# Optimization experiments

Measured on AMD Instinct MI355X. Metric: run time of the kernel, lower is better.

Reference implementation:

```python
import jax, jax.numpy as jnp
import numpy as np

H, B, N, D = 8, 256, 200, 128
KD = D // H                      # key_dim = embed_dim // n_heads = 16
TRI = N * (N - 1) // 2           # strictly upper-triangular count per matrix
NORM = 1.0 / np.sqrt(KD)
NEG = -jnp.inf


def setup_inputs() -> dict:
    key = jax.random.key(0)
    k1, k2, k3, k4, k5 = jax.random.split(key, 5)
    q = jax.random.normal(k1, (B, N, D), dtype=jnp.float32)
    che_mask = jax.random.randint(k2, (H, B, TRI), 0, 2).astype(bool)
    exchange = jax.random.randint(k3, (B, 2), 0, N)
    stdv = 1.0 / np.sqrt(KD)
    Wq = jax.random.uniform(k4, (H, D, KD), jnp.float32, -stdv, stdv)
    Wk = jax.random.uniform(k5, (H, D, KD), jnp.float32, -stdv, stdv)
    return {"q": q, "che_mask": che_mask, "exchange": exchange, "Wq": Wq, "Wk": Wk}


def reference(q, che_mask, exchange, Wq, Wk):
    # Q, K: (H, B, N, KD)
    Q = jnp.einsum('bnd,hdk->hbnk', q, Wq)
    K = jnp.einsum('bnd,hdk->hbnk', q, Wk)
    # tanh-rescaled scores: (H, B, N, N)
    comp = jnp.tanh(NORM * jnp.einsum('hbik,hbjk->hbij', Q, K)) * 10.0

    # 1) lower triangle (incl. diagonal) -> -inf
    tril = jnp.tril(jnp.ones((N, N), dtype=bool))
    comp = jnp.where(tril, NEG, comp)

    # 2) strictly-upper positions where che_mask == 0 -> -inf
    # torch boolean indexing enumerates ~tril elements row-major == triu_indices order
    iu0, iu1 = np.triu_indices(N, k=1)
    keep = jnp.zeros((H, B, N, N), dtype=bool).at[:, :, iu0, iu1].set(che_mask)
    comp = jnp.where(jnp.logical_and(~tril, ~keep), NEG, comp)

    # 3) last 28 query rows fully masked
    comp = comp.at[:, :, -28:, :].set(NEG)

    # 4) per-batch exchange-pair scatter on head 0 only
    b_idx = jnp.arange(B)
    comp = comp.at[0, b_idx, exchange[:, 1], exchange[:, 0]].set(NEG)
    comp = comp.at[0, b_idx, exchange[:, 0], exchange[:, 1]].set(NEG)

    # 5) fixed column 100 masked
    comp = comp.at[:, :, :, 100].set(NEG)

    # global (flattened over N*N) softmax / log_softmax per (head, batch)
    im = comp.reshape(H, B, N * N)
    return jax.nn.log_softmax(im, axis=-1), jax.nn.softmax(im, axis=-1)
```

## Files before the change

### kernel.cpp

```cpp
#include <hip/hip_runtime.h>
#include <math.h>

#define Hh 8
#define Bb 256
#define Nn 200
#define Dd 128
#define KDk 16
#define TRI_ 19900
#define NN_ 40000
#define OUT_HALF 81920000ull
#define QK_FLOATS 6553600

#define NEG_FIN (-1.0e30f)

__device__ __forceinline__ float fast_exp2(float x) {
#if __has_builtin(__builtin_amdgcn_exp2f)
  return __builtin_amdgcn_exp2f(x);
#else
  return exp2f(x);
#endif
}
__device__ __forceinline__ float fast_log2(float x) {
#if __has_builtin(__builtin_amdgcn_logf)
  return __builtin_amdgcn_logf(x);
#else
  return log2f(x);
#endif
}
__device__ __forceinline__ float fast_rcp(float x) {
#if __has_builtin(__builtin_amdgcn_rcpf)
  return __builtin_amdgcn_rcpf(x);
#else
  return 1.0f / x;
#endif
}

__device__ __forceinline__ float dot16(float4 a0, float4 a1, float4 a2, float4 a3,
                                       float4 b0, float4 b1, float4 b2, float4 b3) {
  return a0.x*b0.x + a0.y*b0.y + a0.z*b0.z + a0.w*b0.w
       + a1.x*b1.x + a1.y*b1.y + a1.z*b1.z + a1.w*b1.w
       + a2.x*b2.x + a2.y*b2.y + a2.z*b2.z + a2.w*b2.w
       + a3.x*b3.x + a3.y*b3.y + a3.z*b3.z + a3.w*b3.w;
}

__global__ void k_detect(const unsigned char* __restrict__ che, int* __restrict__ flag) {
  const int t = threadIdx.x;
  unsigned char a4 = 0, a8 = 0;
  #pragma unroll
  for (int k = 0; k < 16; ++k) {
    const int i = t * 16 + k;
    const unsigned char v = che[i];
    if (i & 3) a4 |= v;
    else if (i & 7) a8 |= v;
  }
  const unsigned long long m4 = __ballot(a4 != 0);
  const unsigned long long m8 = __ballot(a8 != 0);
  if (t == 0) *flag = m4 ? 1 : (m8 ? 4 : 8);
}

__global__ __launch_bounds__(256) void k_proj(const float* __restrict__ q,
    const float* __restrict__ Wq, const float* __restrict__ Wk,
    float* __restrict__ Qg, float* __restrict__ Kg) {
  __shared__ float As[64 * 132];
  __shared__ float Bst[128 * 68];
  const int tid = threadIdx.x;
  const int r0 = blockIdx.x * 64;
  const int c0 = blockIdx.y * 64;

  const float4* src = (const float4*)q;
  #pragma unroll
  for (int p = 0; p < 8; ++p) {
    const int t2 = tid + p * 256;
    const int row = t2 >> 5, q4 = t2 & 31;
    float4 v = src[(size_t)(r0 + row) * 32 + q4];
    *(float4*)&As[row * 132 + q4 * 4] = v;
  }
  #pragma unroll
  for (int p = 0; p < 32; ++p) {
    const int t2 = tid + p * 256;
    const int d = t2 >> 6, cl = t2 & 63;
    const int c = c0 + cl;
    const int h = c >> 5, m = (c >> 4) & 1, kk = c & 15;
    const float* Wsrc = m ? Wk : Wq;
    Bst[d * 68 + cl] = Wsrc[(h * 128 + d) * 16 + kk];
  }
  __syncthreads();

  const int tn = tid >> 4;
  const int tc = tid & 15;
  float acc[4][4] = {};
  #pragma unroll
  for (int dq = 0; dq < 32; ++dq) {
    float a[4][4];
    #pragma unroll
    for (int r = 0; r < 4; ++r) {
      float4 t = *(const float4*)&As[(tn * 4 + r) * 132 + dq * 4];
      a[r][0] = t.x; a[r][1] = t.y; a[r][2] = t.z; a[r][3] = t.w;
    }
    #pragma unroll
    for (int dd = 0; dd < 4; ++dd) {
      float4 bv = *(const float4*)&Bst[(dq * 4 + dd) * 68 + tc * 4];
      #pragma unroll
      for (int r = 0; r < 4; ++r) {
        acc[r][0] += a[r][dd] * bv.x;
        acc[r][1] += a[r][dd] * bv.y;
        acc[r][2] += a[r][dd] * bv.z;
        acc[r][3] += a[r][dd] * bv.w;
      }
    }
  }
  const int cq = c0 + tc * 4;
  const int h = cq >> 5, m = (cq >> 4) & 1, kkb = cq & 15;
  float* dst = m ? Kg : Qg;
  #pragma unroll
  for (int r = 0; r < 4; ++r) {
    const int nrow = r0 + tn * 4 + r;
    const int b = nrow / 200, n = nrow - b * 200;
    float4 v = make_float4(acc[r][0], acc[r][1], acc[r][2], acc[r][3]);
    *(float4*)(dst + (size_t)((h * 256 + b) * 200 + n) * 16 + kkb) = v;
  }
}

__global__ __launch_bounds__(512, 4) void k_attn(
    const float* __restrict__ Qg, const float* __restrict__ Kg,
    const unsigned char* __restrict__ che, const int* __restrict__ exch,
    const int* __restrict__ flag, float* __restrict__ out) {
  const int hb = blockIdx.x;
  const int h = hb >> 8, b = hb & 255;
  const int tid = threadIdx.x;
  const int lane = tid & 63;
  const int wave = __builtin_amdgcn_readfirstlane(tid >> 6);
  const int i0 = wave * 25;
  const float* __restrict__ Qb = Qg + (size_t)hb * 3200;
  const float* __restrict__ Kb = Kg + (size_t)hb * 3200;
  const int cs = *flag;
  const unsigned char* __restrict__ cheB = che + (size_t)hb * TRI_ * (size_t)cs;
  const int e0 = exch[2 * b], e1 = exch[2 * b + 1];
  const int h0 = (h == 0) ? 1 : 0;

  __shared__ float red[8];
  __shared__ float c3lds[8 * 25 * 8];

  const float C2E = 0.72134752044448f;
  const float L2E = 1.44269504088896f;

  float acc[25][3];
  #pragma unroll
  for (int c = 0; c < 3; ++c) {
    const int j = lane + (c << 6);
    const float4* kp = (const float4*)(Kb + j * 16);
    const float4 k0 = kp[0], k1 = kp[1], k2 = kp[2], k3 = kp[3];
    #pragma unroll
    for (int r = 0; r < 25; ++r) {
      const float4* qp = (const float4*)(Qb + (i0 + r) * 16);
      acc[r][c] = dot16(qp[0], qp[1], qp[2], qp[3], k0, k1, k2, k3);
    }
  }
  const int j3 = 192 + (lane & 7);
  const float4* kp3 = (const float4*)(Kb + j3 * 16);
  const float4 k30 = kp3[0], k31 = kp3[1], k32 = kp3[2], k33 = kp3[3];

  float psum = 0.0f;
  #pragma unroll
  for (int r = 0; r < 25; ++r) {
    const int i = i0 + r;
    const int rowv = (i < 172) ? 1 : 0;
    const int base = i * 199 - ((i * (i - 1)) >> 1) - i - 1;
    #pragma unroll
    for (int c = 0; c < 4; ++c) {
      int j; float d;
      if (c < 3) {
        j = lane + (c << 6);
        d = acc[r][c];
      } else {
        j = j3;
        const float4* qp = (const float4*)(Qb + i * 16);
        d = dot16(qp[0], qp[1], qp[2], qp[3], k30, k31, k32, k33);
      }
      int geo = rowv & ((j > i) ? 1 : 0) & ((j != 100) ? 1 : 0);
      if (c == 3) geo &= (lane < 8) ? 1 : 0;
      const int idx = geo ? (base + j) : 0;
      const unsigned char mb = cheB[(size_t)idx * (size_t)cs];
      int valid = geo & ((mb != 0) ? 1 : 0);
      const int exhit = (((i == e1) & (j == e0)) | ((i == e0) & (j == e1))) ? 1 : 0;
      valid &= (h0 & exhit) ^ 1;
      const float E = fast_exp2(C2E * d);
      const float rc = fast_rcp(E + 1.0f);
      const float s10 = valid ? (-20.0f * rc) : NEG_FIN;
      psum += fast_exp2(L2E * s10);
      if (c < 3) acc[r][c] = s10;
      else if (lane < 8) c3lds[wave * 200 + r * 8 + lane] = s10;
    }
  }

  #pragma unroll
  for (int o = 32; o > 0; o >>= 1) psum += __shfl_xor(psum, o, 64);
  if (lane == 0) red[wave] = psum;
  __syncthreads();
  float Z = 0.0f;
  #pragma unroll
  for (int w2 = 0; w2 < 8; ++w2) Z += red[w2];
  const float lnZ = 0.69314718056f * fast_log2(Z);

  const size_t obase = (size_t)hb * NN_;
  float* __restrict__ oLS = out + obase;
  float* __restrict__ oSM = out + OUT_HALF + obase;
  #pragma unroll
  for (int r = 0; r < 25; ++r) {
    const int ro = (i0 + r) * 200;
    #pragma unroll
    for (int c = 0; c < 3; ++c) {
      const int j = lane + (c << 6);
      const float ls = acc[r][c] - lnZ;
      const float sm = fast_exp2(L2E * ls);
      oLS[ro + j] = ls;
      oSM[ro + j] = sm;
    }
    {
      const float s10 = c3lds[wave * 200 + r * 8 + (lane & 7)];
      const float ls = s10 - lnZ;
      const float sm = fast_exp2(L2E * ls);
      if (lane < 8) {
        oLS[ro + j3] = ls;
        oSM[ro + j3] = sm;
      }
    }
  }
}

extern "C" void kernel_launch(void* const* d_in, const int* in_sizes, int n_in,
                              void* d_out, int out_size, void* d_ws, size_t ws_size,
                              hipStream_t stream) {
  const float* q           = (const float*)d_in[0];
  const unsigned char* che = (const unsigned char*)d_in[1];
  const int* exch          = (const int*)d_in[2];
  const float* Wq          = (const float*)d_in[3];
  const float* Wk          = (const float*)d_in[4];
  float* out = (float*)d_out;
  float* ws  = (float*)d_ws;

  const size_t need = (size_t)(4 + 2 * QK_FLOATS) * sizeof(float);
  int* flag = (int*)ws;
  float* Qg = ws + 4;
  float* Kg = Qg + QK_FLOATS;

  if (ws_size < need) {
    k_detect<<<dim3(1), dim3(64), 0, stream>>>(che, flag);
    return;
  }

  k_detect<<<dim3(1), dim3(64), 0, stream>>>(che, flag);
  k_proj<<<dim3(800, 4), dim3(256), 0, stream>>>(q, Wq, Wk, Qg, Kg);
  k_attn<<<dim3(2048), dim3(512), 0, stream>>>(Qg, Kg, che, exch, flag, out);
}
```

Measured before the change: 1.087 ms.

## Compute only live upper-triangle segments via work table and store masked regions directly

Replaces the per-wave row blocks with a compile-time table of (row, 64-column segment) work items covering only the strictly upper triangle of the 172 live rows. Dot products, tanh and mask reads now run only for those items, and the lower triangle and dead rows are written as constants. The block grows to 16 waves of 1024 threads and outputs use nontemporal stores. In exchange, the Q/K dot products are recomputed per item instead of reusing register tiles, and the larger block may lower occupancy.

```diff
diff --git a/kernel.cpp b/kernel.cpp
--- a/kernel.cpp
+++ b/kernel.cpp
@@ -13,6 +13,10 @@
 
 #define NEG_FIN (-1.0e30f)
 
+#define NITEMS 385
+#define NWAVES 16
+#define ITEMS_PER_WAVE 25
+
 __device__ __forceinline__ float fast_exp2(float x) {
 #if __has_builtin(__builtin_amdgcn_exp2f)
   return __builtin_amdgcn_exp2f(x);
@@ -42,6 +46,20 @@
        + a2.x*b2.x + a2.y*b2.y + a2.z*b2.z + a2.w*b2.w
        + a3.x*b3.x + a3.y*b3.y + a3.z*b3.z + a3.w*b3.w;
 }
+
+struct ItemTab { unsigned int v[NWAVES * ITEMS_PER_WAVE]; };
+static constexpr ItemTab make_tab() {
+  ItemTab t{};
+  int n = 0;
+  for (int i = 0; i < 172; ++i) {
+    int len = 199 - i;
+    int g = (len + 63) >> 6;
+    for (int k = 0; k < g; ++k) { t.v[n] = (unsigned int)((i << 2) | k); ++n; }
+  }
+  for (; n < NWAVES * ITEMS_PER_WAVE; ++n) t.v[n] = 0xFFFFu;
+  return t;
+}
+__constant__ ItemTab d_tab = make_tab();
 
 __global__ void k_detect(const unsigned char* __restrict__ che, int* __restrict__ flag) {
   const int t = threadIdx.x;
@@ -121,7 +139,7 @@
   }
 }
 
-__global__ __launch_bounds__(512, 4) void k_attn(
+__global__ __launch_bounds__(1024, 4) void k_attn(
     const float* __restrict__ Qg, const float* __restrict__ Kg,
     const unsigned char* __restrict__ che, const int* __restrict__ exch,
     const int* __restrict__ flag, float* __restrict__ out) {
@@ -130,67 +148,44 @@
   const int tid = threadIdx.x;
   const int lane = tid & 63;
   const int wave = __builtin_amdgcn_readfirstlane(tid >> 6);
-  const int i0 = wave * 25;
   const float* __restrict__ Qb = Qg + (size_t)hb * 3200;
   const float* __restrict__ Kb = Kg + (size_t)hb * 3200;
   const int cs = *flag;
-  const unsigned char* __restrict__ cheB = che + (size_t)hb * TRI_ * (size_t)cs;
+  const unsigned char* __restrict__ cheB = che + (size_t)hb * (size_t)TRI_ * (size_t)cs;
   const int e0 = exch[2 * b], e1 = exch[2 * b + 1];
-  const int h0 = (h == 0) ? 1 : 0;
-
-  __shared__ float red[8];
-  __shared__ float c3lds[8 * 25 * 8];
+  const int emin = min(e0, e1), emax = max(e0, e1);
+  const bool h0 = (h == 0);
+
+  __shared__ float red[NWAVES];
 
   const float C2E = 0.72134752044448f;
   const float L2E = 1.44269504088896f;
 
-  float acc[25][3];
-  #pragma unroll
-  for (int c = 0; c < 3; ++c) {
-    const int j = lane + (c << 6);
-    const float4* kp = (const float4*)(Kb + j * 16);
+  float sreg[ITEMS_PER_WAVE];
+  float psum = 0.0f;
+
+  #pragma unroll
+  for (int s = 0; s < ITEMS_PER_WAVE; ++s) {
+    const int iv = (int)d_tab.v[wave * ITEMS_PER_WAVE + s];
+    const int i = iv >> 2;
+    const int g = iv & 3;
+    const int ic = (i < 172) ? i : 0;
+    const int j = i + 1 + (g << 6) + lane;
+    const int jc = (j < 200) ? j : 0;
+    int live = ((j < 200) & (j != 100) & (i < 172)) ? 1 : 0;
+    const int base = ic * 199 - ((ic * (ic - 1)) >> 1) - ic - 1;
+    const int idx = live ? (base + j) : 0;
+    live &= (cheB[(size_t)idx * (size_t)cs] != 0) ? 1 : 0;
+    if (h0 && (i == emin) && (j == emax)) live = 0;
+    const float4* kp = (const float4*)(Kb + jc * 16);
     const float4 k0 = kp[0], k1 = kp[1], k2 = kp[2], k3 = kp[3];
-    #pragma unroll
-    for (int r = 0; r < 25; ++r) {
-      const float4* qp = (const float4*)(Qb + (i0 + r) * 16);
-      acc[r][c] = dot16(qp[0], qp[1], qp[2], qp[3], k0, k1, k2, k3);
-    }
-  }
-  const int j3 = 192 + (lane & 7);
-  const float4* kp3 = (const float4*)(Kb + j3 * 16);
-  const float4 k30 = kp3[0], k31 = kp3[1], k32 = kp3[2], k33 = kp3[3];
-
-  float psum = 0.0f;
-  #pragma unroll
-  for (int r = 0; r < 25; ++r) {
-    const int i = i0 + r;
-    const int rowv = (i < 172) ? 1 : 0;
-    const int base = i * 199 - ((i * (i - 1)) >> 1) - i - 1;
-    #pragma unroll
-    for (int c = 0; c < 4; ++c) {
-      int j; float d;
-      if (c < 3) {
-        j = lane + (c << 6);
-        d = acc[r][c];
-      } else {
-        j = j3;
-        const float4* qp = (const float4*)(Qb + i * 16);
-        d = dot16(qp[0], qp[1], qp[2], qp[3], k30, k31, k32, k33);
-      }
-      int geo = rowv & ((j > i) ? 1 : 0) & ((j != 100) ? 1 : 0);
-      if (c == 3) geo &= (lane < 8) ? 1 : 0;
-      const int idx = geo ? (base + j) : 0;
-      const unsigned char mb = cheB[(size_t)idx * (size_t)cs];
-      int valid = geo & ((mb != 0) ? 1 : 0);
-      const int exhit = (((i == e1) & (j == e0)) | ((i == e0) & (j == e1))) ? 1 : 0;
-      valid &= (h0 & exhit) ^ 1;
-      const float E = fast_exp2(C2E * d);
-      const float rc = fast_rcp(E + 1.0f);
-      const float s10 = valid ? (-20.0f * rc) : NEG_FIN;
-      psum += fast_exp2(L2E * s10);
-      if (c < 3) acc[r][c] = s10;
-      else if (lane < 8) c3lds[wave * 200 + r * 8 + lane] = s10;
-    }
+    const float4* qp = (const float4*)(Qb + ic * 16);
+    const float d = dot16(qp[0], qp[1], qp[2], qp[3], k0, k1, k2, k3);
+    const float E = fast_exp2(C2E * d);
+    const float rc = fast_rcp(E + 1.0f);
+    const float s10 = live ? (-20.0f * rc) : NEG_FIN;
+    psum += fast_exp2(L2E * s10);
+    sreg[s] = s10;
   }
 
   #pragma unroll
@@ -199,30 +194,37 @@
   __syncthreads();
   float Z = 0.0f;
   #pragma unroll
-  for (int w2 = 0; w2 < 8; ++w2) Z += red[w2];
+  for (int w2 = 0; w2 < NWAVES; ++w2) Z += red[w2];
   const float lnZ = 0.69314718056f * fast_log2(Z);
 
   const size_t obase = (size_t)hb * NN_;
   float* __restrict__ oLS = out + obase;
   float* __restrict__ oSM = out + OUT_HALF + obase;
-  #pragma unroll
-  for (int r = 0; r < 25; ++r) {
-    const int ro = (i0 + r) * 200;
+
+  #pragma unroll
+  for (int s = 0; s < ITEMS_PER_WAVE; ++s) {
+    const int iv = (int)d_tab.v[wave * ITEMS_PER_WAVE + s];
+    const int i = iv >> 2;
+    const int g = iv & 3;
+    const int j = i + 1 + (g << 6) + lane;
+    if ((i < 172) && (j < 200)) {
+      const float ls = sreg[s] - lnZ;
+      const float sm = fast_exp2(L2E * ls);
+      const int o = i * 200 + j;
+      __builtin_nontemporal_store(ls, &oLS[o]);
+      __builtin_nontemporal_store(sm, &oSM[o]);
+    }
+  }
+
+  for (int r = wave; r < 200; r += NWAVES) {
+    const int lim = (r < 172) ? r : 199;
     #pragma unroll
-    for (int c = 0; c < 3; ++c) {
-      const int j = lane + (c << 6);
-      const float ls = acc[r][c] - lnZ;
-      const float sm = fast_exp2(L2E * ls);
-      oLS[ro + j] = ls;
-      oSM[ro + j] = sm;
-    }
-    {
-      const float s10 = c3lds[wave * 200 + r * 8 + (lane & 7)];
-      const float ls = s10 - lnZ;
-      const float sm = fast_exp2(L2E * ls);
-      if (lane < 8) {
-        oLS[ro + j3] = ls;
-        oSM[ro + j3] = sm;
+    for (int gc = 0; gc < 4; ++gc) {
+      const int j = (gc << 6) + lane;
+      if (j <= lim && j < 200) {
+        const int o = r * 200 + j;
+        __builtin_nontemporal_store(NEG_FIN, &oLS[o]);
+        __builtin_nontemporal_store(0.0f, &oSM[o]);
       }
     }
   }
@@ -251,5 +253,5 @@
 
   k_detect<<<dim3(1), dim3(64), 0, stream>>>(che, flag);
   k_proj<<<dim3(800, 4), dim3(256), 0, stream>>>(q, Wq, Wk, Qg, Kg);
-  k_attn<<<dim3(2048), dim3(512), 0, stream>>>(Qg, Kg, che, exch, flag, out);
-}
+  k_attn<<<dim3(2048), dim3(1024), 0, stream>>>(Qg, Kg, che, exch, flag, out);
+}
```

Result: no change. 1.081 ms (-0.5%).
